# Performance work log

Hardware: AMD Instinct MI355X
Metric: run time of the kernel (lower is better)

## Reference

```python
import jax, jax.numpy as jnp
import numpy as np


def setup_inputs() -> dict:
    key = jax.random.key(0)
    x = jax.random.normal(key, (8, 2048, 3), dtype=jnp.float32)
    return {"x": x, "k": 16}


def reference(x, k):
    b, n, d = x.shape
    xf = x.reshape(b * n, d)                      # flatten across batch, as in the torch module
    sq = jnp.sum(xf * xf, axis=1, keepdims=True)  # [BN, 1]
    pair = 2.0 * (xf @ xf.T) - sq - sq.T          # [BN, BN] = -dist^2
    # torch topk(largest=False) on pair == largest of (-pair) == largest squared distance
    neg_vals, idx = jax.lax.top_k(-pair, k + 1)   # [BN, k+1]
    dists = -neg_vals
    dists = dists[:, 1:].reshape(b, n, k)
    idx = idx[:, 1:].reshape(b, n, k)
    return dists, idx
```

## Files before the change

### kernel.cpp

```cpp
#include <hip/hip_runtime.h>
#include <stdint.h>

#define BN       16384
#define NTILES   256
#define NB       64
#define KOUT     16
#define MARGIN   0.01f

typedef float v2f __attribute__((ext_vector_type(2)));
union F4 { float4 f4; v2f p[2]; float f[4]; };

#define WS_TAB    0
#define WS_IDX    (WS_TAB + BN * 16)
#define WS_BND    (WS_IDX + BN * 4)
#define WS_HIST   (WS_BND + NTILES * 8)
#define WS_HMAX   (WS_HIST + 64 * NB * 4)
#define WS_CBASE  (WS_HMAX + 64 * NB * 4)

__device__ __forceinline__ unsigned key_u(unsigned u) {
    return u ^ ((unsigned)((int)u >> 31) | 0x80000000u);
}
__device__ __forceinline__ unsigned wshr1(unsigned v, unsigned oldv) {
    return (unsigned)__builtin_amdgcn_update_dpp((int)oldv, (int)v, 0x138 ,
                                                 0xF, 0xF, false);
}
#define RL16(T) __uint_as_float((unsigned)__builtin_amdgcn_readlane(__float_as_int(T), 16))

__device__ __forceinline__ float sq_of(float gx, float gy, float gz) {
    return __fadd_rn(__fadd_rn(__fmul_rn(gx, gx), __fmul_rn(gy, gy)), __fmul_rn(gz, gz));
}
__device__ __forceinline__ int bucket_of(float sq) {
    const float rho = __fsqrt_rn(sq);
    int b = (int)(64.0f * (1.0f - rho * 0.2f));
    return (b < 0) ? 0 : ((b > 63) ? 63 : b);
}

#define DRAIN(m, p, jvec, T, J)                                                     \
    while (m) {                                                                     \
        const int b_ = (int)__builtin_ctzll(m);                                     \
        m &= m - 1;                                                                 \
        const float pc_ = __uint_as_float(                                          \
            (unsigned)__builtin_amdgcn_readlane(__float_as_int(p), b_));            \
        const unsigned jc_ = (unsigned)__builtin_amdgcn_readlane((int)(jvec), b_);  \
        const float Tup_ =                                                          \
            __uint_as_float(wshr1(__float_as_uint(T), 0xFF800000u ));       \
        const unsigned Jup_ = wshr1((J), 0u);                                       \
        const bool lt_ = (pc_ < Tup_) || ((pc_ == Tup_) && (jc_ < Jup_));           \
        const float Tn_ = lt_ ? Tup_ : pc_;                                         \
        const unsigned Jn_ = lt_ ? Jup_ : jc_;                                      \
        const bool sel_ = (pc_ < (T)) || ((pc_ == (T)) && (jc_ < (J)));             \
        (T) = sel_ ? Tn_ : (T);                                                     \
        (J) = sel_ ? Jn_ : (J);                                                     \
    }

#define EVALC(c, d2)                                                                \
    asm("v_pk_mul_f32 %0, %1, %2 op_sel:[0,0] op_sel_hi:[0,1]"                      \
        : "=v"(d2) : "v"((c).p[0]), "v"(c0A));                                      \
    asm("v_pk_fma_f32 %0, %1, %2, %0 op_sel:[1,0,0] op_sel_hi:[1,1,1]"              \
        : "+v"(d2) : "v"((c).p[0]), "v"(c1A));                                      \
    asm("v_pk_fma_f32 %0, %1, %2, %0 op_sel:[0,0,0] op_sel_hi:[0,1,1]"              \
        : "+v"(d2) : "v"((c).p[1]), "v"(c2A));                                      \
    asm("v_pk_add_f32 %0, %0, %1" : "+v"(d2) : "v"(nsq01));                         \
    asm("v_pk_add_f32 %0, %0, %1 op_sel:[0,1] op_sel_hi:[1,1]"                      \
        : "+v"(d2) : "v"((c).p[1]));

#define TILE_AT(t)                                                                  \
    F4 c; c.f4 = tab[(t) * 64 + lane];                                              \
    const unsigned jvec = idxarr[(t) * 64 + lane];                                  \
    v2f d2; EVALC(c, d2)

#define PROCESS_LOADED()                                                            \
    do {                                                                            \
        uint64_t m0 = __ballot(d2[0] <= fF0);                                       \
        uint64_t m1 = __ballot(d2[1] <= fF1);                                       \
        if (m0 | m1) {                                                              \
            const float p0 = d2[0], p1 = d2[1];                                     \
            DRAIN(m0, p0, jvec, T0, J0)                                             \
            DRAIN(m1, p1, jvec, T1, J1)                                             \
            fF0 = RL16(T0); thr0 = __fsub_rn(-fF0, MARGIN);                         \
            fF1 = RL16(T1); thr1 = __fsub_rn(-fF1, MARGIN);                         \
        }                                                                           \
    } while (0)

__device__ __forceinline__ void presort64(float p, unsigned j, int lane, double* sw,
                                          float& T, unsigned& J) {
    const double dm = (double)key_u(__float_as_uint(p)) * 16384.0 + (double)j;
    sw[lane] = dm;
    unsigned rank = 0;
    const char* sb = (const char*)sw;
    unsigned off = (unsigned)lane * 8u;
#pragma unroll 7
    for (int s = 1; s < 64; ++s) {
        off = (off + 8u) & 511u;
        const double dn = *(const double*)(sb + off);
        rank += (dn < dm) ? 1u : 0u;
    }
    sw[rank] = __longlong_as_double(
        (long long)(((unsigned long long)j << 32) | __float_as_uint(p)));
    const unsigned long long v = (unsigned long long)__double_as_longlong(sw[lane]);
    T = __uint_as_float((unsigned)(v & 0xFFFFFFFFull));
    J = (unsigned)(v >> 32);
}

__global__ __launch_bounds__(256) void k_hist(const float* __restrict__ x,
                                              unsigned* __restrict__ hist,
                                              unsigned* __restrict__ hmax) {
    __shared__ unsigned h[NB], m[NB];
    const int tid = threadIdx.x;
    if (tid < NB) { h[tid] = 0u; m[tid] = 0u; }
    __syncthreads();
    const int i = blockIdx.x * 256 + tid;
    const float sq = sq_of(x[3 * i], x[3 * i + 1], x[3 * i + 2]);
    const int b = bucket_of(sq);
    atomicAdd(&h[b], 1u);
    atomicMax(&m[b], __float_as_uint(sq));
    __syncthreads();
    if (tid < NB) {
        hist[blockIdx.x * NB + tid] = h[tid];
        hmax[blockIdx.x * NB + tid] = m[tid];
    }
}

__global__ __launch_bounds__(256) void k_mid(const unsigned* __restrict__ hist,
                                             const unsigned* __restrict__ hmax,
                                             unsigned* __restrict__ cbase,
                                             float2* __restrict__ bnd) {
    __shared__ unsigned tot[NB], basev[NB + 1], sfx[NB];
    const int tid = threadIdx.x;
    if (tid < NB) {
        unsigned s = 0, mx = 0;
        for (int g = 0; g < 64; ++g) {
            s += hist[g * NB + tid];
            const unsigned w = hmax[g * NB + tid];
            mx = (w > mx) ? w : mx;
        }
        tot[tid] = s;
        sfx[tid] = mx;
    }
    __syncthreads();
    if (tid == 0) {
        unsigned s = 0;
        for (int b = 0; b < NB; ++b) { basev[b] = s; s += tot[b]; }
        basev[NB] = s;
        unsigned M = 0;
        for (int b = NB - 1; b >= 0; --b) { const unsigned w = sfx[b]; M = (w > M) ? w : M; sfx[b] = M; }
    }
    __syncthreads();
    if (tid < NB) {
        unsigned s = basev[tid];
        for (int g = 0; g < 64; ++g) {
            cbase[g * NB + tid] = s;
            s += hist[g * NB + tid];
        }
    }
    {
        const unsigned pos = (unsigned)tid * 64u;
        int b = 0;
        for (int bb = 0; bb < NB; ++bb)
            if (basev[bb] <= pos && pos < basev[bb + 1]) b = bb;
        const float B = __uint_as_float(sfx[b]);
        const float sqB_up = __uint_as_float(__float_as_uint(__fsqrt_rn(B)) + 2u);
        bnd[tid] = make_float2(B, sqB_up);
    }
}

__global__ __launch_bounds__(256) void k_scatter(const float* __restrict__ x,
                                                 const unsigned* __restrict__ cbase,
                                                 float4* __restrict__ tab,
                                                 unsigned* __restrict__ idxarr) {
    __shared__ unsigned c[NB];
    const int tid = threadIdx.x;
    if (tid < NB) c[tid] = 0u;
    __syncthreads();
    const int i = blockIdx.x * 256 + tid;
    const float gx = x[3 * i], gy = x[3 * i + 1], gz = x[3 * i + 2];
    const float sq = sq_of(gx, gy, gz);
    const int b = bucket_of(sq);
    const unsigned r = atomicAdd(&c[b], 1u);
    const unsigned pos = cbase[blockIdx.x * NB + b] + r;
    tab[pos] = make_float4(gx, gy, gz, -sq);
    idxarr[pos] = (unsigned)i;
}

__global__ __launch_bounds__(256) void knn_far_kernel(
    const float* __restrict__ x, const float4* __restrict__ tab,
    const unsigned* __restrict__ idxarr, const float2* __restrict__ bnd,
    float* __restrict__ out_d, float* __restrict__ out_i) {
    __shared__ double swall[4 * 64];
    const int tid  = threadIdx.x;
    const int lane = tid & 63;
    const int wid  = tid >> 6;
    double* sw = swall + wid * 64;
    const int q0 = (blockIdx.x * 4 + wid) * 2;
    const int q1 = q0 + 1;

    const float a0 = x[3 * q0], a1 = x[3 * q0 + 1], a2 = x[3 * q0 + 2];
    const float b0 = x[3 * q1], b1 = x[3 * q1 + 1], b2 = x[3 * q1 + 2];
    const float sq0 = sq_of(a0, a1, a2), sq1 = sq_of(b0, b1, b2);
    const v2f nsq01 = {-sq0, -sq1};
    const v2f c0A = {2.0f * a0, 2.0f * b0};
    const v2f c1A = {2.0f * a1, 2.0f * b1};
    const v2f c2A = {2.0f * a2, 2.0f * b2};
    const float twor0 = 2.0f * __uint_as_float(__float_as_uint(__fsqrt_rn(sq0)) + 2u);
    const float twor1 = 2.0f * __uint_as_float(__float_as_uint(__fsqrt_rn(sq1)) + 2u);

    float T0, T1; unsigned J0, J1;
    float fF0, fF1, thr0, thr1;

    {
        TILE_AT(0)
        presort64(d2[0], jvec, lane, sw, T0, J0);
        presort64(d2[1], jvec, lane, sw, T1, J1);
        fF0 = RL16(T0); thr0 = __fsub_rn(-fF0, MARGIN);
        fF1 = RL16(T1); thr1 = __fsub_rn(-fF1, MARGIN);
    }
#pragma unroll
    for (int t = 1; t < 4; ++t) {
        TILE_AT(t)
        PROCESS_LOADED();
    }
    for (int t = 4; t < NTILES; ++t) {
        const float2 bd = bnd[t];
        const float u0 = __builtin_fmaf(twor0, bd.y, __fadd_rn(sq0, bd.x));
        const float u1 = __builtin_fmaf(twor1, bd.y, __fadd_rn(sq1, bd.x));
        if (u0 < thr0 && u1 < thr1) break;
        TILE_AT(t)
        PROCESS_LOADED();
    }

    if (lane >= 1 && lane <= KOUT) {
        const int r = lane - 1;
        out_d[q0 * KOUT + r] = T0;
        out_i[q0 * KOUT + r] = (float)J0;
        out_d[q1 * KOUT + r] = T1;
        out_i[q1 * KOUT + r] = (float)J1;
    }
}

extern "C" void kernel_launch(void* const* d_in, const int* in_sizes, int n_in,
                              void* d_out, int out_size, void* d_ws, size_t ws_size,
                              hipStream_t stream) {
    const float* x = (const float*)d_in[0];
    char* ws = (char*)d_ws;
    float4*   tab    = (float4*)(ws + WS_TAB);
    unsigned* idxarr = (unsigned*)(ws + WS_IDX);
    float2*   bnd    = (float2*)(ws + WS_BND);
    unsigned* hist   = (unsigned*)(ws + WS_HIST);
    unsigned* hmax   = (unsigned*)(ws + WS_HMAX);
    unsigned* cbase  = (unsigned*)(ws + WS_CBASE);
    float* out_d = (float*)d_out;
    float* out_i = out_d + (size_t)BN * KOUT;

    hipLaunchKernelGGL(k_hist,    dim3(64), dim3(256), 0, stream, x, hist, hmax);
    hipLaunchKernelGGL(k_mid,     dim3(1),  dim3(256), 0, stream, hist, hmax, cbase, bnd);
    hipLaunchKernelGGL(k_scatter, dim3(64), dim3(256), 0, stream, x, cbase, tab, idxarr);
    hipLaunchKernelGGL(knn_far_kernel, dim3(BN / 8), dim3(256), 0, stream,
                       x, tab, idxarr, bnd, out_d, out_i);
}
```

Before: 83.07 us.

## Fuse prefix-sum into scatter kernel and rank presort with DPP rotates

Removes the single-block k_mid launch. Each scatter block now recomputes the bucket totals and its own per-bucket prefix from the histogram, and block 0 also computes the suffix-max bounds. This saves one kernel launch and one serial single-block stage, at the cost of every block redundantly reading the full histogram. Separately, the 64-element rank sort in presort64 now rotates values across lanes with DPP wave_ror instead of reading them back from LDS, trading LDS traffic for 126 DPP moves per sort.

```diff
diff --git a/kernel.cpp b/kernel.cpp
--- a/kernel.cpp
+++ b/kernel.cpp
@@ -15,7 +15,6 @@
 #define WS_BND    (WS_IDX + BN * 4)
 #define WS_HIST   (WS_BND + NTILES * 8)
 #define WS_HMAX   (WS_HIST + 64 * NB * 4)
-#define WS_CBASE  (WS_HMAX + 64 * NB * 4)
 
 __device__ __forceinline__ unsigned key_u(unsigned u) {
     return u ^ ((unsigned)((int)u >> 31) | 0x80000000u);
@@ -23,6 +22,13 @@
 __device__ __forceinline__ unsigned wshr1(unsigned v, unsigned oldv) {
     return (unsigned)__builtin_amdgcn_update_dpp((int)oldv, (int)v, 0x138 ,
                                                  0xF, 0xF, false);
+}
+__device__ __forceinline__ double wror1_f64(double v) {
+    const unsigned long long u = (unsigned long long)__double_as_longlong(v);
+    unsigned lo = (unsigned)u, hi = (unsigned)(u >> 32);
+    lo = (unsigned)__builtin_amdgcn_update_dpp((int)lo, (int)lo, 0x13C, 0xF, 0xF, false);
+    hi = (unsigned)__builtin_amdgcn_update_dpp((int)hi, (int)hi, 0x13C, 0xF, 0xF, false);
+    return __longlong_as_double((long long)(((unsigned long long)hi << 32) | lo));
 }
 #define RL16(T) __uint_as_float((unsigned)__builtin_amdgcn_readlane(__float_as_int(T), 16))
 
@@ -85,15 +91,12 @@
 __device__ __forceinline__ void presort64(float p, unsigned j, int lane, double* sw,
                                           float& T, unsigned& J) {
     const double dm = (double)key_u(__float_as_uint(p)) * 16384.0 + (double)j;
-    sw[lane] = dm;
+    double rot = dm;
     unsigned rank = 0;
-    const char* sb = (const char*)sw;
-    unsigned off = (unsigned)lane * 8u;
-#pragma unroll 7
-    for (int s = 1; s < 64; ++s) {
-        off = (off + 8u) & 511u;
-        const double dn = *(const double*)(sb + off);
-        rank += (dn < dm) ? 1u : 0u;
+#pragma unroll
+    for (int s = 0; s < 63; ++s) {
+        rot = wror1_f64(rot);
+        rank += (rot < dm) ? 1u : 0u;
     }
     sw[rank] = __longlong_as_double(
         (long long)(((unsigned long long)j << 32) | __float_as_uint(p)));
@@ -121,65 +124,63 @@
     }
 }
 
-__global__ __launch_bounds__(256) void k_mid(const unsigned* __restrict__ hist,
-                                             const unsigned* __restrict__ hmax,
-                                             unsigned* __restrict__ cbase,
-                                             float2* __restrict__ bnd) {
-    __shared__ unsigned tot[NB], basev[NB + 1], sfx[NB];
+__global__ __launch_bounds__(256) void k_scatter(const float* __restrict__ x,
+                                                 const unsigned* __restrict__ hist,
+                                                 const unsigned* __restrict__ hmax,
+                                                 float4* __restrict__ tab,
+                                                 unsigned* __restrict__ idxarr,
+                                                 float2* __restrict__ bnd) {
+    __shared__ unsigned tot_s[NB], pre_s[NB], basev[NB + 1], c[NB], sfx[NB];
     const int tid = threadIdx.x;
+    const int g0 = (int)blockIdx.x;
     if (tid < NB) {
-        unsigned s = 0, mx = 0;
+        unsigned s = 0, pre = 0;
         for (int g = 0; g < 64; ++g) {
-            s += hist[g * NB + tid];
-            const unsigned w = hmax[g * NB + tid];
-            mx = (w > mx) ? w : mx;
+            const unsigned hh = hist[g * NB + tid];
+            pre += (g < g0) ? hh : 0u;
+            s += hh;
         }
-        tot[tid] = s;
-        sfx[tid] = mx;
+        tot_s[tid] = s;
+        pre_s[tid] = pre;
+        if (g0 == 0) {
+            unsigned mx = 0;
+            for (int g = 0; g < 64; ++g) {
+                const unsigned w = hmax[g * NB + tid];
+                mx = (w > mx) ? w : mx;
+            }
+            sfx[tid] = mx;
+        }
     }
     __syncthreads();
     if (tid == 0) {
         unsigned s = 0;
-        for (int b = 0; b < NB; ++b) { basev[b] = s; s += tot[b]; }
+        for (int b = 0; b < NB; ++b) { basev[b] = s; s += tot_s[b]; }
         basev[NB] = s;
-        unsigned M = 0;
-        for (int b = NB - 1; b >= 0; --b) { const unsigned w = sfx[b]; M = (w > M) ? w : M; sfx[b] = M; }
-    }
-    __syncthreads();
-    if (tid < NB) {
-        unsigned s = basev[tid];
-        for (int g = 0; g < 64; ++g) {
-            cbase[g * NB + tid] = s;
-            s += hist[g * NB + tid];
+        if (g0 == 0) {
+            unsigned M = 0;
+            for (int b = NB - 1; b >= 0; --b) {
+                const unsigned w = sfx[b]; M = (w > M) ? w : M; sfx[b] = M;
+            }
         }
     }
-    {
-        const unsigned pos = (unsigned)tid * 64u;
-        int b = 0;
-        for (int bb = 0; bb < NB; ++bb)
-            if (basev[bb] <= pos && pos < basev[bb + 1]) b = bb;
-        const float B = __uint_as_float(sfx[b]);
-        const float sqB_up = __uint_as_float(__float_as_uint(__fsqrt_rn(B)) + 2u);
-        bnd[tid] = make_float2(B, sqB_up);
-    }
-}
-
-__global__ __launch_bounds__(256) void k_scatter(const float* __restrict__ x,
-                                                 const unsigned* __restrict__ cbase,
-                                                 float4* __restrict__ tab,
-                                                 unsigned* __restrict__ idxarr) {
-    __shared__ unsigned c[NB];
-    const int tid = threadIdx.x;
-    if (tid < NB) c[tid] = 0u;
-    __syncthreads();
-    const int i = blockIdx.x * 256 + tid;
+    __syncthreads();
+    if (tid < NB) c[tid] = basev[tid] + pre_s[tid];
+    __syncthreads();
+    const int i = g0 * 256 + tid;
     const float gx = x[3 * i], gy = x[3 * i + 1], gz = x[3 * i + 2];
     const float sq = sq_of(gx, gy, gz);
     const int b = bucket_of(sq);
-    const unsigned r = atomicAdd(&c[b], 1u);
-    const unsigned pos = cbase[blockIdx.x * NB + b] + r;
+    const unsigned pos = atomicAdd(&c[b], 1u);
     tab[pos] = make_float4(gx, gy, gz, -sq);
     idxarr[pos] = (unsigned)i;
+    if (g0 == 0) {
+        const unsigned posn = (unsigned)tid * 64u;
+        int b2 = 0;
+        for (int bb = 0; bb < NB; ++bb) b2 = (basev[bb] <= posn) ? bb : b2;
+        const float B = __uint_as_float(sfx[b2]);
+        const float sqB_up = __uint_as_float(__float_as_uint(__fsqrt_rn(B)) + 2u);
+        bnd[tid] = make_float2(B, sqB_up);
+    }
 }
 
 __global__ __launch_bounds__(256) void knn_far_kernel(
@@ -247,13 +248,12 @@
     float2*   bnd    = (float2*)(ws + WS_BND);
     unsigned* hist   = (unsigned*)(ws + WS_HIST);
     unsigned* hmax   = (unsigned*)(ws + WS_HMAX);
-    unsigned* cbase  = (unsigned*)(ws + WS_CBASE);
     float* out_d = (float*)d_out;
     float* out_i = out_d + (size_t)BN * KOUT;
 
     hipLaunchKernelGGL(k_hist,    dim3(64), dim3(256), 0, stream, x, hist, hmax);
-    hipLaunchKernelGGL(k_mid,     dim3(1),  dim3(256), 0, stream, hist, hmax, cbase, bnd);
-    hipLaunchKernelGGL(k_scatter, dim3(64), dim3(256), 0, stream, x, cbase, tab, idxarr);
+    hipLaunchKernelGGL(k_scatter, dim3(64), dim3(256), 0, stream, x, hist, hmax,
+                       tab, idxarr, bnd);
     hipLaunchKernelGGL(knn_far_kernel, dim3(BN / 8), dim3(256), 0, stream,
                        x, tab, idxarr, bnd, out_d, out_i);
 }
```

Result: no change. 83.18 us (+0.1%).
